# Kernel optimization log

Measured on AMD Instinct MI355X. Metric: run time of the kernel, lower is better.

## Reference

```python
import jax, jax.numpy as jnp
import numpy as np


def _gcn_conv(x, src, dst, W, b, n_nodes):
    # PyG GCNConv: add self-loops, symmetric normalization D^-1/2 A D^-1/2,
    # linear transform, scatter-add aggregation, bias.
    loop = jnp.arange(n_nodes, dtype=src.dtype)
    s = jnp.concatenate([src, loop])
    d = jnp.concatenate([dst, loop])
    deg = jax.ops.segment_sum(jnp.ones_like(s, dtype=x.dtype), d, num_segments=n_nodes)
    dinv = jnp.where(deg > 0, jax.lax.rsqrt(deg), 0.0)
    norm = dinv[s] * dinv[d]                      # [E+N]
    h = x @ W                                     # [N, H] dense GEMM
    msg = h[s] * norm[:, None]                    # [E+N, H] gathered messages
    out = jax.ops.segment_sum(msg, d, num_segments=n_nodes)  # scatter-add
    return out + b


def setup_inputs() -> dict:
    key = jax.random.key(0)
    ks = jax.random.split(key, 8)
    n_nodes, n_edges, d_in, hidden, num_graphs = 10000, 160000, 512, 512, 64
    x = jax.random.normal(ks[0], (n_nodes, d_in), dtype=jnp.float32)
    edge_index = jax.random.randint(ks[1], (2, n_edges), 0, n_nodes, dtype=jnp.int64)
    batch = jnp.sort(jax.random.randint(ks[2], (n_nodes,), 0, num_graphs, dtype=jnp.int64))
    # Xavier-uniform-ish weights (GCNConv lin has no bias separate in newer PyG; keep W+b per layer)
    def xavier(k, shape):
        fan_in, fan_out = shape[0], shape[1]
        lim = np.sqrt(6.0 / (fan_in + fan_out))
        return jax.random.uniform(k, shape, jnp.float32, -lim, lim)
    W1 = xavier(ks[3], (d_in, hidden))
    b1 = jnp.zeros((hidden,), jnp.float32)
    W2 = xavier(ks[4], (hidden, hidden))
    b2 = jnp.zeros((hidden,), jnp.float32)
    Wlin = xavier(ks[5], (hidden, 1))
    blin = jnp.zeros((1,), jnp.float32)
    return {"x": x, "edge_index": edge_index, "batch": batch, "num_graphs": num_graphs,
            "W1": W1, "b1": b1, "W2": W2, "b2": b2, "Wlin": Wlin, "blin": blin}


def reference(x, edge_index, batch, num_graphs, W1, b1, W2, b2, Wlin, blin):
    n_nodes = x.shape[0]
    src, dst = edge_index[0], edge_index[1]
    h = _gcn_conv(x, src, dst, W1, b1, n_nodes)
    h = jax.nn.relu(h)
    h = _gcn_conv(h, src, dst, W2, b2, n_nodes)
    pooled = jax.ops.segment_sum(h, batch, num_segments=num_graphs)  # global_add_pool
    return pooled @ Wlin + blin  # [num_graphs, 1]
```

## Files before the change

### kernel.cpp

```cpp
#include <hip/hip_runtime.h>
#include <stdint.h>

typedef __attribute__((ext_vector_type(8))) short s16x8;
typedef __attribute__((ext_vector_type(8))) unsigned short u16x8;
typedef __attribute__((ext_vector_type(4))) float f32x4;

#define D 512
#define BM 128
#define BK 64
#define CAP 96

__device__ __forceinline__ unsigned short f2bf(float f) {
    unsigned u = __float_as_uint(f);
    return (unsigned short)((u + 0x7FFFu + ((u >> 16) & 1u)) >> 16);
}
__device__ __forceinline__ float bf2f(unsigned short h) {
    return __uint_as_float(((unsigned)h) << 16);
}

__global__ __launch_bounds__(256) void k_prep(const float* W1, int* fill, float* z,
                                              unsigned short* w1t, int nN) {
    int b = blockIdx.x, t = threadIdx.x;
    if (b < 64) {
        __shared__ float tile[64][65];
        int ti = b >> 3, tj = b & 7;
#pragma unroll
        for (int p = 0; p < 4; ++p) {
            int r = p * 16 + (t >> 4);
            int c = (t & 15) * 4;
            float4 v = *(const float4*)(W1 + (size_t)(ti * 64 + r) * D + tj * 64 + c);
            tile[r][c] = v.x; tile[r][c + 1] = v.y; tile[r][c + 2] = v.z; tile[r][c + 3] = v.w;
        }
        __syncthreads();
        int c = t >> 2;
        int r0 = (t & 3) * 16;
        u16x8 o0, o1;
#pragma unroll
        for (int i = 0; i < 8; ++i) o0[i] = f2bf(tile[r0 + i][c]);
#pragma unroll
        for (int i = 0; i < 8; ++i) o1[i] = f2bf(tile[r0 + 8 + i][c]);
        unsigned short* wp = w1t + (size_t)(tj * 64 + c) * D + ti * 64 + r0;
        *(u16x8*)wp = o0;
        *(u16x8*)(wp + 8) = o1;
    } else {
        int i = (b - 64) * 256 + t;
        if (i < nN) { fill[i] = 0; z[i] = 0.f; }
    }
}

__global__ __launch_bounds__(256) void k_gemm_scatter(const float* X, const unsigned short* BT,
                                                      unsigned short* C, int Mreal,
                                                      const int* src, const int* dst,
                                                      int* fill, int* csr_src, int nE,
                                                      const float* W2, const float* Wlin,
                                                      const float* b2, const float* blin,
                                                      float* w2l, float* out, int nG) {
    __shared__ __align__(16) unsigned short smem[128 * 132];
    unsigned short* As = smem;
    unsigned short* Bs = smem + BM * BK;
    int b = blockIdx.x;
    int t = threadIdx.x;
    if (b >= 316) {
        int br = b - 316;
        if (br < 625) {
            int e = br * 256 + t;
            if (e < nE) {
                int s = src[e], d = dst[e];
                int pos = atomicAdd(&fill[d], 1);
                if (pos < CAP) csr_src[(size_t)d * CAP + pos] = s;
            }
        } else if (br < 754) {
            int i = (br - 625) * 4 + (t >> 6);
            int l = t & 63;
            if (i < D + 1) {
                const float* row = (i < D) ? (W2 + (size_t)i * D) : b2;
                float4 a0 = *(const float4*)(row + l * 8);
                float4 a1 = *(const float4*)(row + l * 8 + 4);
                float4 c0 = *(const float4*)(Wlin + l * 8);
                float4 c1 = *(const float4*)(Wlin + l * 8 + 4);
                float p = a0.x * c0.x + a0.y * c0.y + a0.z * c0.z + a0.w * c0.w
                        + a1.x * c1.x + a1.y * c1.y + a1.z * c1.z + a1.w * c1.w;
#pragma unroll
                for (int o = 32; o > 0; o >>= 1) p += __shfl_xor(p, o);
                if (l == 0) w2l[i] = p;
            }
        } else {
            if (t < nG) out[t] = blin[0];
        }
        return;
    }
    int tn0 = (b & 3) * BM, tm0 = (b >> 2) * BM;
    int lane = t & 63, wave = t >> 6;
    int wr = wave >> 1, wc = wave & 1;
    f32x4 acc[4][4] = {};
    int r15 = lane & 15;
    int khalf = lane >> 4;

    for (int k0 = 0; k0 < D; k0 += BK) {
        __syncthreads();
        {
            int rb0 = wave * 8;
#pragma unroll
            for (int c = 0; c < 4; ++c) {
                int rbase = c * 32 + rb0;
                int row = rbase + (lane >> 3);
                int kg = (lane & 7) ^ (row & 7);
                const unsigned short* gsrc = BT + (size_t)(tn0 + row) * D + k0 + kg * 8;
                __builtin_amdgcn_global_load_lds(
                    (const __attribute__((address_space(1))) unsigned int*)gsrc,
                    (__attribute__((address_space(3))) unsigned int*)(Bs + rbase * BK),
                    16, 0, 0);
            }
        }
#pragma unroll
        for (int i = 0; i < 4; ++i) {
            int idx = t + 256 * i;
            int row = idx >> 3, kg = idx & 7;
            int grow = tm0 + row; if (grow >= Mreal) grow = Mreal - 1;
            const float* gp = X + (size_t)grow * D + k0 + kg * 8;
            float4 f0 = *(const float4*)gp;
            float4 f1 = *(const float4*)(gp + 4);
            u16x8 o;
            o[0] = f2bf(f0.x); o[1] = f2bf(f0.y); o[2] = f2bf(f0.z); o[3] = f2bf(f0.w);
            o[4] = f2bf(f1.x); o[5] = f2bf(f1.y); o[6] = f2bf(f1.z); o[7] = f2bf(f1.w);
            *(u16x8*)&As[row * BK + (kg ^ (row & 7)) * 8] = o;
        }
        __syncthreads();
#pragma unroll
        for (int ks = 0; ks < 2; ++ks) {
            int g = ks * 4 + khalf;
            s16x8 a[4], bb[4];
#pragma unroll
            for (int m = 0; m < 4; ++m) {
                int row = wr * 64 + m * 16 + r15;
                a[m] = *(const s16x8*)&As[row * BK + (g ^ (row & 7)) * 8];
            }
#pragma unroll
            for (int n = 0; n < 4; ++n) {
                int row = wc * 64 + n * 16 + r15;
                bb[n] = *(const s16x8*)&Bs[row * BK + (g ^ (row & 7)) * 8];
            }
#pragma unroll
            for (int m = 0; m < 4; ++m)
#pragma unroll
                for (int n = 0; n < 4; ++n)
                    acc[m][n] = __builtin_amdgcn_mfma_f32_16x16x32_bf16(a[m], bb[n], acc[m][n], 0, 0, 0);
        }
    }

    __syncthreads();
    int cr = (lane >> 4) * 4;
    int cc = lane & 15;
#pragma unroll
    for (int m = 0; m < 4; ++m)
#pragma unroll
        for (int n = 0; n < 4; ++n)
#pragma unroll
            for (int r = 0; r < 4; ++r)
                smem[(wr * 64 + m * 16 + cr + r) * 132 + wc * 64 + n * 16 + cc] = f2bf(acc[m][n][r]);
    __syncthreads();
#pragma unroll
    for (int it = 0; it < 8; ++it) {
        int row = it * 16 + (t >> 4);
        int c8 = (t & 15) * 8;
        int grow = tm0 + row;
        if (grow < Mreal) {
            u16x8 vv = *(const u16x8*)&smem[row * 132 + c8];
            *(u16x8*)&C[(size_t)grow * D + tn0 + c8] = vv;
        }
    }
}

__global__ __launch_bounds__(256) void k_agg1(const unsigned short* h1b, const int* csr_src,
                                              const int* fill, const float* b1,
                                              const float* w2l, float* z, int nN) {
    int bid = blockIdx.x;
    int xcd = bid & 7;
    int slice = xcd >> 1;
    int chunk = (bid >> 3) * 2 + (xcd & 1);
    int t = threadIdx.x;
    int g = t >> 4;
    int l = t & 15;
    int v = chunk * 16 + g;
    if (v >= nN) return;
    int f0 = (slice << 7) + l * 8;

    float acc[8];
    float4 ba = *(const float4*)(b1 + f0);
    float4 bb = *(const float4*)(b1 + f0 + 4);
    acc[0] = ba.x; acc[1] = ba.y; acc[2] = ba.z; acc[3] = ba.w;
    acc[4] = bb.x; acc[5] = bb.y; acc[6] = bb.z; acc[7] = bb.w;

    int deg = fill[v];
    float degv1 = (float)(deg + 1);
    float wself = 1.0f / degv1;
    u16x8 hv = *(const u16x8*)(h1b + (size_t)v * D + f0);
#pragma unroll
    for (int j = 0; j < 8; ++j) acc[j] += wself * bf2f(hv[j]);

    const int* row = csr_src + (size_t)v * CAP;
    int sb = (g & 3) << 4;
    for (int eb = 0; eb < deg; eb += 16) {
        int n = deg - eb; if (n > 16) n = 16;
        int myi = 0; float myw = 0.f;
        if (l < n) {
            myi = row[eb + l];
            myw = rsqrtf((float)(fill[myi] + 1) * degv1);
        }
        int j = 0;
        for (; j + 4 <= n; j += 4) {
            int s0 = __shfl(myi, sb + j),     s1 = __shfl(myi, sb + j + 1);
            int s2 = __shfl(myi, sb + j + 2), s3 = __shfl(myi, sb + j + 3);
            float w0 = __shfl(myw, sb + j),     w1 = __shfl(myw, sb + j + 1);
            float w2 = __shfl(myw, sb + j + 2), w3 = __shfl(myw, sb + j + 3);
            u16x8 h0 = *(const u16x8*)(h1b + (size_t)s0 * D + f0);
            u16x8 h1 = *(const u16x8*)(h1b + (size_t)s1 * D + f0);
            u16x8 h2 = *(const u16x8*)(h1b + (size_t)s2 * D + f0);
            u16x8 h3 = *(const u16x8*)(h1b + (size_t)s3 * D + f0);
#pragma unroll
            for (int q = 0; q < 8; ++q) acc[q] += w0 * bf2f(h0[q]);
#pragma unroll
            for (int q = 0; q < 8; ++q) acc[q] += w1 * bf2f(h1[q]);
#pragma unroll
            for (int q = 0; q < 8; ++q) acc[q] += w2 * bf2f(h2[q]);
#pragma unroll
            for (int q = 0; q < 8; ++q) acc[q] += w3 * bf2f(h3[q]);
        }
        for (; j < n; ++j) {
            int s = __shfl(myi, sb + j);
            float w = __shfl(myw, sb + j);
            u16x8 hs = *(const u16x8*)(h1b + (size_t)s * D + f0);
#pragma unroll
            for (int q = 0; q < 8; ++q) acc[q] += w * bf2f(hs[q]);
        }
    }

    float4 wa = *(const float4*)(w2l + f0);
    float4 wb = *(const float4*)(w2l + f0 + 4);
    float wv[8] = {wa.x, wa.y, wa.z, wa.w, wb.x, wb.y, wb.z, wb.w};
    float p = 0.f;
#pragma unroll
    for (int j = 0; j < 8; ++j) p += fmaxf(acc[j], 0.f) * wv[j];
    p += __shfl_xor(p, 8);
    p += __shfl_xor(p, 4);
    p += __shfl_xor(p, 2);
    p += __shfl_xor(p, 1);
    if (l == 0) atomicAdd(&z[v], p);
}

__global__ __launch_bounds__(256) void k_agg2(const float* z, const int* src, const int* dst,
                                              const int* fill, const float* w2l,
                                              const int* batch, float* out, int nN, int nE, int nG) {
    __shared__ float bins[64];
    int t = threadIdx.x;
    if (t < 64) bins[t] = 0.f;
    __syncthreads();
    int i = blockIdx.x * 256 + t;
    if (i < nE) {
        int s = src[i], d = dst[i];
        float val = rsqrtf((float)(fill[s] + 1) * (float)(fill[d] + 1)) * z[s];
        int g = batch[d];
        if (g < 64) atomicAdd(&bins[g], val); else atomicAdd(&out[g], val);
    }
    if (i < nN) {
        float val = w2l[D] + z[i] / (float)(fill[i] + 1);
        int g = batch[i];
        if (g < 64) atomicAdd(&bins[g], val); else atomicAdd(&out[g], val);
    }
    __syncthreads();
    if (t < 64 && t < nG) {
        float v = bins[t];
        if (v != 0.f) atomicAdd(&out[t], v);
    }
}

extern "C" void kernel_launch(void* const* d_in, const int* in_sizes, int n_in,
                              void* d_out, int out_size, void* d_ws, size_t ws_size,
                              hipStream_t stream) {
    const float* x    = (const float*)d_in[0];
    const int*   ei   = (const int*)d_in[1];
    const int*   batch= (const int*)d_in[2];
    const float* W1   = (const float*)d_in[4];
    const float* b1   = (const float*)d_in[5];
    const float* W2   = (const float*)d_in[6];
    const float* b2   = (const float*)d_in[7];
    const float* Wlin = (const float*)d_in[8];
    const float* blin = (const float*)d_in[9];
    float* out = (float*)d_out;

    int nN = in_sizes[0] / D;
    int nE = in_sizes[1] / 2;
    int nG = out_size;
    const int* src = ei;
    const int* dst = ei + nE;

    char* p = (char*)d_ws;
    auto alloc = [&](size_t b) { char* r = p; p += (b + 255) & ~(size_t)255; return (void*)r; };
    int*   fill    = (int*)alloc((size_t)nN * 4);
    int*   csr_src = (int*)alloc((size_t)nN * CAP * 4);
    float* z       = (float*)alloc((size_t)nN * 4);
    float* w2l     = (float*)alloc((size_t)(D + 1) * 4);
    unsigned short* w1t = (unsigned short*)alloc((size_t)D * D * 2);
    unsigned short* h1b = (unsigned short*)alloc((size_t)nN * D * 2);

    k_prep<<<104, 256, 0, stream>>>(W1, fill, z, w1t, nN);
    int nb = 316 + (nE + 255) / 256 + 129 + 1;
    k_gemm_scatter<<<nb, 256, 0, stream>>>(x, w1t, h1b, nN, src, dst, fill, csr_src, nE,
                                           W2, Wlin, b2, blin, w2l, out, nG);
    k_agg1<<<313 * 8, 256, 0, stream>>>(h1b, csr_src, fill, b1, w2l, z, nN);
    nb = (nE + 255) / 256;
    k_agg2<<<nb, 256, 0, stream>>>(z, src, dst, fill, w2l, batch, out, nN, nE, nG);
}
```

Baseline: 69.51 us.

## Double-buffer GEMM tiles to prefetch next K-slice during MFMA compute

After: 67.97 us, median of 2. 2.2% less time.

```diff
diff --git a/kernel.cpp b/kernel.cpp
--- a/kernel.cpp
+++ b/kernel.cpp
@@ -55,9 +55,7 @@
                                                       const float* W2, const float* Wlin,
                                                       const float* b2, const float* blin,
                                                       float* w2l, float* out, int nG) {
-    __shared__ __align__(16) unsigned short smem[128 * 132];
-    unsigned short* As = smem;
-    unsigned short* Bs = smem + BM * BK;
+    __shared__ __align__(16) unsigned short smem[4 * BM * BK];
     int b = blockIdx.x;
     int t = threadIdx.x;
     if (b >= 316) {
@@ -96,36 +94,63 @@
     int r15 = lane & 15;
     int khalf = lane >> 4;
 
+    int a_row[4], a_kg[4];
+    const float* a_gp_base[4];
+#pragma unroll
+    for (int i = 0; i < 4; ++i) {
+        int idx = t + 256 * i;
+        a_row[i] = idx >> 3; a_kg[i] = idx & 7;
+        int grow = tm0 + a_row[i]; if (grow >= Mreal) grow = Mreal - 1;
+        a_gp_base[i] = X + (size_t)grow * D + a_kg[i] * 8;
+    }
+
+    auto issue_B = [&](unsigned short* Bsbuf, int k0) {
+        int rb0 = wave * 8;
+#pragma unroll
+        for (int c = 0; c < 4; ++c) {
+            int rbase = c * 32 + rb0;
+            int row = rbase + (lane >> 3);
+            int kg = (lane & 7) ^ (row & 7);
+            const unsigned short* gsrc = BT + (size_t)(tn0 + row) * D + k0 + kg * 8;
+            __builtin_amdgcn_global_load_lds(
+                (const __attribute__((address_space(1))) unsigned int*)gsrc,
+                (__attribute__((address_space(3))) unsigned int*)(Bsbuf + rbase * BK),
+                16, 0, 0);
+        }
+    };
+
+    float4 af0[4], af1[4];
+    auto load_A = [&](int k0) {
+#pragma unroll
+        for (int i = 0; i < 4; ++i) {
+            const float* gp = a_gp_base[i] + k0;
+            af0[i] = *(const float4*)gp;
+            af1[i] = *(const float4*)(gp + 4);
+        }
+    };
+    auto write_A = [&](unsigned short* Asbuf) {
+#pragma unroll
+        for (int i = 0; i < 4; ++i) {
+            u16x8 o;
+            o[0] = f2bf(af0[i].x); o[1] = f2bf(af0[i].y); o[2] = f2bf(af0[i].z); o[3] = f2bf(af0[i].w);
+            o[4] = f2bf(af1[i].x); o[5] = f2bf(af1[i].y); o[6] = f2bf(af1[i].z); o[7] = f2bf(af1[i].w);
+            *(u16x8*)&Asbuf[a_row[i] * BK + (a_kg[i] ^ (a_row[i] & 7)) * 8] = o;
+        }
+    };
+
+    issue_B(smem + 2 * BM * BK, 0);
+    load_A(0);
+    write_A(smem);
+    __syncthreads();
+
+    int cur = 0;
     for (int k0 = 0; k0 < D; k0 += BK) {
-        __syncthreads();
-        {
-            int rb0 = wave * 8;
-#pragma unroll
-            for (int c = 0; c < 4; ++c) {
-                int rbase = c * 32 + rb0;
-                int row = rbase + (lane >> 3);
-                int kg = (lane & 7) ^ (row & 7);
-                const unsigned short* gsrc = BT + (size_t)(tn0 + row) * D + k0 + kg * 8;
-                __builtin_amdgcn_global_load_lds(
-                    (const __attribute__((address_space(1))) unsigned int*)gsrc,
-                    (__attribute__((address_space(3))) unsigned int*)(Bs + rbase * BK),
-                    16, 0, 0);
-            }
-        }
-#pragma unroll
-        for (int i = 0; i < 4; ++i) {
-            int idx = t + 256 * i;
-            int row = idx >> 3, kg = idx & 7;
-            int grow = tm0 + row; if (grow >= Mreal) grow = Mreal - 1;
-            const float* gp = X + (size_t)grow * D + k0 + kg * 8;
-            float4 f0 = *(const float4*)gp;
-            float4 f1 = *(const float4*)(gp + 4);
-            u16x8 o;
-            o[0] = f2bf(f0.x); o[1] = f2bf(f0.y); o[2] = f2bf(f0.z); o[3] = f2bf(f0.w);
-            o[4] = f2bf(f1.x); o[5] = f2bf(f1.y); o[6] = f2bf(f1.z); o[7] = f2bf(f1.w);
-            *(u16x8*)&As[row * BK + (kg ^ (row & 7)) * 8] = o;
-        }
-        __syncthreads();
+        unsigned short* Asc = smem + cur * BM * BK;
+        unsigned short* Bsc = smem + (2 + cur) * BM * BK;
+        if (k0 + BK < D) {
+            issue_B(smem + (2 + (cur ^ 1)) * BM * BK, k0 + BK);
+            load_A(k0 + BK);
+        }
 #pragma unroll
         for (int ks = 0; ks < 2; ++ks) {
             int g = ks * 4 + khalf;
@@ -133,12 +158,12 @@
 #pragma unroll
             for (int m = 0; m < 4; ++m) {
                 int row = wr * 64 + m * 16 + r15;
-                a[m] = *(const s16x8*)&As[row * BK + (g ^ (row & 7)) * 8];
+                a[m] = *(const s16x8*)&Asc[row * BK + (g ^ (row & 7)) * 8];
             }
 #pragma unroll
             for (int n = 0; n < 4; ++n) {
                 int row = wc * 64 + n * 16 + r15;
-                bb[n] = *(const s16x8*)&Bs[row * BK + (g ^ (row & 7)) * 8];
+                bb[n] = *(const s16x8*)&Bsc[row * BK + (g ^ (row & 7)) * 8];
             }
 #pragma unroll
             for (int m = 0; m < 4; ++m)
@@ -146,9 +171,11 @@
                 for (int n = 0; n < 4; ++n)
                     acc[m][n] = __builtin_amdgcn_mfma_f32_16x16x32_bf16(a[m], bb[n], acc[m][n], 0, 0, 0);
         }
-    }
-
-    __syncthreads();
+        if (k0 + BK < D) write_A(smem + (cur ^ 1) * BM * BK);
+        __syncthreads();
+        cur ^= 1;
+    }
+
     int cr = (lane >> 4) * 4;
     int cc = lane & 15;
 #pragma unroll
```
